# Kernel tuning notes

Measured on AMD Instinct MI355X. Metric: run time of the kernel, lower is better.

The kernel has to match this reference:

```python
import jax, jax.numpy as jnp
import numpy as np

NQ = 8
N = 2 ** NQ
NCYC = 4
B = 8192
_POP = np.array([bin(i).count('1') for i in range(N)], dtype=np.float32)  # popcount per basis state
_CNOT = np.array([[1, 0, 0, 0], [0, 1, 0, 0], [0, 0, 0, 1], [0, 0, 1, 0]], dtype=np.complex64)
_I4 = np.eye(4, dtype=np.complex64)
_XX = np.fliplr(np.eye(4)).astype(np.complex64)  # X (x) X in the 2-qubit basis


def _apply1(psi, U, w):
    # single-qubit gate U (2x2) on wire w; psi: (B, 256)
    b = psi.shape[0]
    s = psi.reshape(b, 1 << w, 2, -1)
    return jnp.einsum('ij,bljr->blir', U, s).reshape(b, N)


def _apply2_adj_b(psi, U, w):
    # batched 4x4 gate U (B,4,4) on adjacent wires (w, w+1)
    b = psi.shape[0]
    s = psi.reshape(b, 1 << w, 4, -1)
    return jnp.einsum('bij,bljr->blir', U, s).reshape(b, N)


def _apply2(psi, U, w0, w1):
    # fixed 4x4 gate on arbitrary wires (w0, w1)
    b = psi.shape[0]
    t = psi.reshape((b,) + (2,) * NQ)
    t = jnp.tensordot(jnp.asarray(U).reshape(2, 2, 2, 2), t, axes=((2, 3), (w0 + 1, w1 + 1)))
    t = jnp.moveaxis(t, (0, 1), (w0 + 1, w1 + 1))
    return t.reshape(b, N)


def _rz_mat(t):
    e = jnp.exp(-0.5j * t)
    return jnp.diag(jnp.stack([e, jnp.conj(e)])).astype(jnp.complex64)


def _ry_mat(t):
    c = jnp.cos(0.5 * t)
    s = jnp.sin(0.5 * t)
    return jnp.stack([jnp.stack([c, -s]), jnp.stack([s, c])]).astype(jnp.complex64)


def _u3_mat(p):
    th, ph, la = p[0], p[1], p[2]
    cc = jnp.cos(0.5 * th).astype(jnp.complex64)
    ss = jnp.sin(0.5 * th).astype(jnp.complex64)
    r0 = jnp.stack([cc, -jnp.exp(1j * la) * ss])
    r1 = jnp.stack([jnp.exp(1j * ph) * ss, jnp.exp(1j * (ph + la)) * cc])
    return jnp.stack([r0, r1]).astype(jnp.complex64)


def _expz(psi, w):
    # <Z_w> = p(bit=0) - p(bit=1)
    b = psi.shape[0]
    p = jnp.abs(psi.reshape(b, 1 << w, 2, -1)) ** 2
    m = p.sum(axis=(1, 3))
    return m[:, 0] - m[:, 1]


def _conv(psi, rz3, ry2, wq, wp):
    # RZ(wq) CNOT(wq,wp) RZ(wp) RY(wq) CNOT(wp,wq) RY(wq) CNOT(wq,wp) RZ(wp)
    psi = _apply1(psi, _rz_mat(rz3[0]), wq)
    psi = _apply2(psi, _CNOT, wq, wp)
    psi = _apply1(psi, _rz_mat(rz3[1]), wp)
    psi = _apply1(psi, _ry_mat(ry2[0]), wq)
    psi = _apply2(psi, _CNOT, wp, wq)
    psi = _apply1(psi, _ry_mat(ry2[1]), wq)
    psi = _apply2(psi, _CNOT, wq, wp)
    psi = _apply1(psi, _rz_mat(rz3[2]), wp)
    return psi


def setup_inputs() -> dict:
    key = jax.random.key(0)
    ks = jax.random.split(key, 8)
    pi = np.float32(np.pi)
    theta = jax.random.uniform(ks[0], (B,), jnp.float32, 0.0, pi / 2)
    phi = jax.random.uniform(ks[1], (B,), jnp.float32, 0.0, pi / 2)
    rz_params = jax.random.uniform(ks[2], (21,), jnp.float32, -pi, pi)
    ry_params = jax.random.uniform(ks[3], (14,), jnp.float32, -pi, pi)
    u3_params = jax.random.uniform(ks[4], (6, 3), jnp.float32, -pi, pi)
    w1 = jax.random.normal(ks[5], (10, 2), jnp.float32) / np.sqrt(2.0).astype(np.float32)
    b1 = jnp.zeros((10,), jnp.float32)
    w2 = jax.random.normal(ks[6], (1, 10), jnp.float32) / np.sqrt(10.0).astype(np.float32)
    b2 = jnp.zeros((1,), jnp.float32)
    return {'theta': theta, 'phi': phi, 'rz_params': rz_params, 'ry_params': ry_params,
            'u3_params': u3_params, 'w1': w1, 'b1': b1, 'w2': w2, 'b2': b2}


def reference(theta, phi, rz_params, ry_params, u3_params, w1, b1, w2, b2):
    b = theta.shape[0]
    # H on every wire from |0...0> -> uniform amplitudes 1/sqrt(2^8)
    psi = jnp.full((b, N), np.float32(2.0 ** (-NQ / 2)), dtype=jnp.complex64)
    # rz(2*phi) on all 8 wires == diagonal phase exp(i*phi*(2*popcount - 8))
    zphase = jnp.exp(1j * phi[:, None] * (2.0 * _POP[None, :] - NQ)).astype(jnp.complex64)
    # rxx(2*theta): cos(theta) I - i sin(theta) XX, batched over angles
    c = jnp.cos(theta)
    s = jnp.sin(theta)
    Urxx = (c[:, None, None] * _I4 - 1j * s[:, None, None] * _XX).astype(jnp.complex64)
    for _ in range(NCYC):
        psi = psi * zphase
        for w in (0, 2, 4, 6):  # pairs (0,1),(2,3),(4,5),(6,7)
            psi = _apply2_adj_b(psi, Urxx, w)
        for w in (1, 3, 5):  # pairs (1,2),(3,4),(5,6)
            psi = _apply2_adj_b(psi, Urxx, w)
    # first conv layer on pairs (1,0),(3,2),(5,4),(7,6)
    for i, (wq, wp) in enumerate([(1, 0), (3, 2), (5, 4), (7, 6)]):
        psi = _conv(psi, rz_params[3 * i:3 * i + 3], ry_params[2 * i:2 * i + 2], wq, wp)
    # U3 pooling on wires 1,3,5,7
    for i, w in enumerate((1, 3, 5, 7)):
        psi = _apply1(psi, _u3_mat(u3_params[i]), w)
    # second conv layer on pairs (3,1),(7,5),(5,3)
    for j, (wq, wp) in enumerate([(3, 1), (7, 5), (5, 3)]):
        i = 4 + j
        psi = _conv(psi, rz_params[3 * i:3 * i + 3], ry_params[2 * i:2 * i + 2], wq, wp)
    psi = _apply1(psi, _u3_mat(u3_params[4]), 3)
    psi = _apply1(psi, _u3_mat(u3_params[5]), 7)
    feats = jnp.stack([_expz(psi, 3), _expz(psi, 7)], axis=-1)  # (B, 2)
    h = jnp.tanh(feats @ w1.T + b1)
    return jax.nn.sigmoid(h @ w2.T + b2)  # (B, 1)
```

## Files before the change

kernel.cpp:

```cpp
#include <hip/hip_runtime.h>

typedef float2 cplx;

__device__ __forceinline__ cplx cmul(cplx a, cplx b){
  return make_float2(a.x*b.x - a.y*b.y, a.x*b.y + a.y*b.x);
}
__device__ __forceinline__ cplx cmad(cplx a, cplx b, cplx acc){
  return make_float2(acc.x + a.x*b.x - a.y*b.y, acc.y + a.x*b.y + a.y*b.x);
}

__device__ __forceinline__ void rz_gate(cplx* st, float t, int bmask){
  float s, c; sincosf(0.5f*t, &s, &c);
  cplx em = make_float2(c, -s), ep = make_float2(c, s);
  for(int k=0;k<4;k++) st[k] = cmul(st[k], (k & bmask) ? ep : em);
}
__device__ __forceinline__ void ry_gate_q(cplx* st, float t){
  float s, c; sincosf(0.5f*t, &s, &c);
  for(int bp=0;bp<2;bp++){
    cplx a0 = st[bp], a1 = st[2+bp];
    st[bp]   = make_float2(c*a0.x - s*a1.x, c*a0.y - s*a1.y);
    st[2+bp] = make_float2(s*a0.x + c*a1.x, s*a0.y + c*a1.y);
  }
}
__device__ __forceinline__ void u3_gate(cplx* st, const float* p, int onq){
  float th=p[0], ph=p[1], la=p[2];
  float ss,cc,sl,cl,sp,cp,spl,cpl;
  sincosf(0.5f*th,&ss,&cc); sincosf(la,&sl,&cl); sincosf(ph,&sp,&cp); sincosf(ph+la,&spl,&cpl);
  cplx u00=make_float2(cc,0.f), u01=make_float2(-cl*ss,-sl*ss);
  cplx u10=make_float2(cp*ss,sp*ss), u11=make_float2(cpl*cc,spl*cc);
  if(onq){
    for(int bp=0;bp<2;bp++){
      cplx a0=st[bp], a1=st[2+bp];
      st[bp]   = cmad(u01,a1,cmul(u00,a0));
      st[2+bp] = cmad(u11,a1,cmul(u10,a0));
    }
  } else {
    for(int bq=0;bq<2;bq++){
      cplx a0=st[2*bq], a1=st[2*bq+1];
      st[2*bq]   = cmad(u01,a1,cmul(u00,a0));
      st[2*bq+1] = cmad(u11,a1,cmul(u10,a0));
    }
  }
}


#define DPP_XOR1 0xB1
#define DPP_XOR2 0x4E
#define DPP_XOR3 0x1B
#define DPP_ROR8 0x128

template<int C>
__device__ __forceinline__ float xdpp(float x){
  return __builtin_bit_cast(float,
    __builtin_amdgcn_mov_dpp(__builtin_bit_cast(int, x), C, 0xF, 0xF, true));
}
template<int MASK>
__device__ __forceinline__ float xswz(float x){
  return __builtin_bit_cast(float,
    __builtin_amdgcn_ds_swizzle(__builtin_bit_cast(int, x), (MASK<<10) | 0x1F));
}

enum Sh { SH_DPP1, SH_DPP2, SH_DPP3, SH_ROR8, SH_SWZ4, SH_SWZ6, SH_SWZ10, SH_SWZ12 };

template<Sh S> __device__ __forceinline__ float shf(float x){
  if      constexpr(S==SH_DPP1)  return xdpp<DPP_XOR1>(x);
  else if constexpr(S==SH_DPP2)  return xdpp<DPP_XOR2>(x);
  else if constexpr(S==SH_DPP3)  return xdpp<DPP_XOR3>(x);
  else if constexpr(S==SH_ROR8)  return xdpp<DPP_ROR8>(x);
  else if constexpr(S==SH_SWZ4)  return xswz<4>(x);
  else if constexpr(S==SH_SWZ6)  return xswz<6>(x);
  else if constexpr(S==SH_SWZ10) return xswz<10>(x);
  else                           return xswz<12>(x);
}
template<Sh S> __device__ __forceinline__ cplx shc(cplx a){
  return make_float2(shf<S>(a.x), shf<S>(a.y));
}

template<int MR>
__device__ __forceinline__ void rxx_reg(cplx* v, float c, float s){
  #pragma unroll
  for(int r=0;r<16;r++){
    int q = r ^ MR;
    if(r > q) continue;
    cplx a = v[r], b = v[q];
    v[r] = make_float2(c*a.x + s*b.y, c*a.y - s*b.x);
    v[q] = make_float2(c*b.x + s*a.y, c*b.y - s*a.x);
  }
}
template<Sh S>
__device__ __forceinline__ void rxx_lane(cplx* v, float c, float s){
  #pragma unroll
  for(int r=0;r<16;r++){
    cplx p = shc<S>(v[r]);
    v[r] = make_float2(c*v[r].x + s*p.y, c*v[r].y - s*p.x);
  }
}
__device__ __forceinline__ void rxx_mix34(cplx* v, float c, float s){
  #pragma unroll
  for(int r=0;r<16;r+=2){
    cplx pa = shc<SH_DPP1>(v[r^1]);
    cplx pb = shc<SH_DPP1>(v[r]);
    cplx a = v[r], b = v[r^1];
    v[r]   = make_float2(c*a.x + s*pa.y, c*a.y - s*pa.x);
    v[r^1] = make_float2(c*b.x + s*pb.y, c*b.y - s*pb.x);
  }
}

template<int MQ, int MP>
__device__ __forceinline__ void conv_reg(cplx* v, const cplx* M){
  #pragma unroll
  for(int r=0;r<16;r++){
    if((r & (MQ|MP)) != 0) continue;
    cplx a0=v[r], a1=v[r^MP], a2=v[r^MQ], a3=v[r^MQ^MP];
    v[r]        = cmad(M[3], a3, cmad(M[2], a2, cmad(M[1], a1, cmul(M[0], a0))));
    v[r^MP]     = cmad(M[7], a3, cmad(M[6], a2, cmad(M[5], a1, cmul(M[4], a0))));
    v[r^MQ]     = cmad(M[11],a3, cmad(M[10],a2, cmad(M[9], a1, cmul(M[8], a0))));
    v[r^MQ^MP]  = cmad(M[15],a3, cmad(M[14],a2, cmad(M[13],a1, cmul(M[12],a0))));
  }
}

template<Sh SQ, Sh SP, Sh SB>
__device__ __forceinline__ void conv_lane(cplx* v, const cplx* M, int k){
  cplx es = M[k*4 + k], ep = M[k*4 + (k^1)], eq = M[k*4 + (k^2)], eb = M[k*4 + (k^3)];
  #pragma unroll
  for(int r=0;r<16;r++){
    cplx pq = shc<SQ>(v[r]);
    cplx pp = shc<SP>(v[r]);
    cplx pb = shc<SB>(v[r]);
    v[r] = cmad(eb, pb, cmad(eq, pq, cmad(ep, pp, cmul(es, v[r]))));
  }
}

__device__ __forceinline__ void conv_53(cplx* v, const cplx* M, int s1){
  int t = 2*s1, u = 2 - t;
  const cplx* r0 = M + t*4;
  const cplx* r1 = M + (t+1)*4;
  cplx e00=r0[t], e01=r0[t+1], e02=r0[u], e03=r0[u+1];
  cplx e10=r1[t], e11=r1[t+1], e12=r1[u], e13=r1[u+1];
  #pragma unroll
  for(int r=0;r<16;r+=2){
    cplx pv0 = shc<SH_DPP2>(v[r]);
    cplx pv1 = shc<SH_DPP2>(v[r+1]);
    cplx a0 = v[r], a1 = v[r+1];
    v[r]   = cmad(e03, pv1, cmad(e02, pv0, cmad(e01, a1, cmul(e00, a0))));
    v[r+1] = cmad(e13, pv1, cmad(e12, pv0, cmad(e11, a1, cmul(e10, a0))));
  }
}

__global__ void __launch_bounds__(256) qcnn_kernel(
    const float* __restrict__ theta, const float* __restrict__ phi,
    const float* __restrict__ rz, const float* __restrict__ ry,
    const float* __restrict__ u3,
    const float* __restrict__ w1, const float* __restrict__ b1,
    const float* __restrict__ w2, const float* __restrict__ b2,
    float* __restrict__ out){
  __shared__ cplx Msh[112];

  int tid  = threadIdx.x;

  if(tid < 28){
    int ci = tid >> 2, col = tid & 3;
    const float* rz3 = rz + 3*ci;
    const float* ry2 = ry + 2*ci;
    int u3slot = 0, u3idx = 0;
    if(ci <= 3){ u3slot = 1; u3idx = ci; }
    else if(ci == 5){ u3slot = 1; u3idx = 5; }
    else if(ci == 6){ u3slot = 2; u3idx = 4; }
    cplx st[4];
    for(int k=0;k<4;k++) st[k] = make_float2(k==col ? 1.f : 0.f, 0.f);
    rz_gate(st, rz3[0], 2);
    { cplx tmp=st[2]; st[2]=st[3]; st[3]=tmp; }
    rz_gate(st, rz3[1], 1);
    ry_gate_q(st, ry2[0]);
    { cplx tmp=st[1]; st[1]=st[3]; st[3]=tmp; }
    ry_gate_q(st, ry2[1]);
    { cplx tmp=st[2]; st[2]=st[3]; st[3]=tmp; }
    rz_gate(st, rz3[2], 1);
    if(u3slot == 1)      u3_gate(st, u3+3*u3idx, 1);
    else if(u3slot == 2) u3_gate(st, u3+3*u3idx, 0);
    for(int k=0;k<4;k++) Msh[ci*16 + k*4 + col] = st[k];
  }
  __syncthreads();

  int s_   = tid & 15;
  int b    = blockIdx.x*16 + (tid >> 4);
  int s0 = s_&1, s1 = (s_>>1)&1, s2 = (s_>>2)&1, s3 = (s_>>3)&1;

  float th = theta[b], ph = phi[b];
  float c, s;
  __sincosf(th, &s, &c);

  cplx zp[5];
  {
    int base = __popc(s_);
    float a0 = ph * (float)(2*base - 8);
    float sa, ca, s2p, c2p;
    __sincosf(a0, &sa, &ca);
    __sincosf(2.f*ph, &s2p, &c2p);
    cplx step = make_float2(c2p, s2p);
    zp[0] = make_float2(ca, sa);
    #pragma unroll
    for(int j=1;j<5;j++) zp[j] = cmul(zp[j-1], step);
  }

  cplx v[16];
  #pragma unroll
  for(int r=0;r<16;r++){
    cplx z = zp[__popc(r)];
    v[r] = make_float2(0.0625f*z.x, 0.0625f*z.y);
  }

  #pragma unroll 1
  for(int cyc=0;cyc<4;cyc++){
    if(cyc){
      #pragma unroll
      for(int r=0;r<16;r++) v[r] = cmul(v[r], zp[__popc(r)]);
    }
    rxx_reg<12>(v, c, s);
    rxx_reg<3>(v, c, s);
    rxx_lane<SH_DPP3>(v, c, s);
    rxx_lane<SH_SWZ12>(v, c, s);
    rxx_reg<6>(v, c, s);
    rxx_mix34(v, c, s);
    rxx_lane<SH_SWZ6>(v, c, s);
  }

  conv_reg<4,8>(v, Msh +  0);
  conv_reg<1,2>(v, Msh + 16);
  conv_lane<SH_DPP2,SH_DPP1,SH_DPP3>(v, Msh + 32, 2*s1 + s0);
  conv_lane<SH_ROR8,SH_SWZ4,SH_SWZ12>(v, Msh + 48, 2*s3 + s2);
  conv_reg<1,4>(v, Msh + 64);
  conv_lane<SH_ROR8,SH_DPP2,SH_SWZ10>(v, Msh + 80, 2*s3 + s1);
  conv_53(v, Msh + 96, s1);

  float tot = 0.f, z3 = 0.f;
  #pragma unroll
  for(int r=0;r<16;r++){
    float m = v[r].x*v[r].x + v[r].y*v[r].y;
    tot += m;
    z3 += (r & 1) ? -m : m;
  }
  float z7 = (s_ & 8) ? -tot : tot;
  z3 += xdpp<DPP_XOR1>(z3);  z7 += xdpp<DPP_XOR1>(z7);
  z3 += xdpp<DPP_XOR2>(z3);  z7 += xdpp<DPP_XOR2>(z7);
  z3 += xswz<4>(z3);         z7 += xswz<4>(z7);
  z3 += xdpp<DPP_ROR8>(z3);  z7 += xdpp<DPP_ROR8>(z7);

  float acc = 0.f;
  if(s_ < 10){
    float hv = tanhf(z3*w1[2*s_] + z7*w1[2*s_+1] + b1[s_]);
    acc = hv * w2[s_];
  }
  acc += xdpp<DPP_XOR1>(acc);
  acc += xdpp<DPP_XOR2>(acc);
  acc += xswz<4>(acc);
  acc += xdpp<DPP_ROR8>(acc);

  if(s_ == 0){
    float a = acc + b2[0];
    out[b] = 1.f / (1.f + __expf(-a));
  }
}

extern "C" void kernel_launch(void* const* d_in, const int* in_sizes, int n_in,
                              void* d_out, int out_size, void* d_ws, size_t ws_size,
                              hipStream_t stream) {
  const float* theta = (const float*)d_in[0];
  const float* phi   = (const float*)d_in[1];
  const float* rz    = (const float*)d_in[2];
  const float* ry    = (const float*)d_in[3];
  const float* u3    = (const float*)d_in[4];
  const float* w1    = (const float*)d_in[5];
  const float* b1    = (const float*)d_in[6];
  const float* w2    = (const float*)d_in[7];
  const float* b2    = (const float*)d_in[8];

  hipLaunchKernelGGL(qcnn_kernel, dim3(8192/16), dim3(256), 0, stream,
                     theta, phi, rz, ry, u3, w1, b1, w2, b2, (float*)d_out);
}
```

Measured before the change: 90.90 us.

## Use packed float2 vector math and replace ds_swizzle with chained DPP moves

Switches the complex type to a native two-float vector so the compiler can emit packed FMA instructions (v_pk_fma_f32) for the gate arithmetic. It also replaces every ds_swizzle cross-lane permutation with a composition of two DPP moves (quad permute followed by row mirror/half-mirror or rotate), so the shuffles avoid the LDS path. The DPP row modifiers address lanes differently from the xor swizzles, so the lane mapping must still give the same xor partners for correctness.

Result: no change. 90.07 us (-0.9%).

```diff
diff --git a/kernel.cpp b/kernel.cpp
--- a/kernel.cpp
+++ b/kernel.cpp
@@ -1,33 +1,40 @@
 #include <hip/hip_runtime.h>
 
-typedef float2 cplx;
-
+typedef float f32x2 __attribute__((ext_vector_type(2)));
+typedef f32x2 cplx;
+
+__device__ __forceinline__ cplx imul(cplx b){
+  cplx r = { -b[1], b[0] }; return r;
+}
 __device__ __forceinline__ cplx cmul(cplx a, cplx b){
-  return make_float2(a.x*b.x - a.y*b.y, a.x*b.y + a.y*b.x);
+  return a.xx*b + a.yy*imul(b);
 }
 __device__ __forceinline__ cplx cmad(cplx a, cplx b, cplx acc){
-  return make_float2(acc.x + a.x*b.x - a.y*b.y, acc.y + a.x*b.y + a.y*b.x);
+  return acc + a.xx*b + a.yy*imul(b);
+}
+__device__ __forceinline__ cplx rxx_upd(float c, cplx a, float s, cplx p){
+  return c*a - s*imul(p);
 }
 
 __device__ __forceinline__ void rz_gate(cplx* st, float t, int bmask){
   float s, c; sincosf(0.5f*t, &s, &c);
-  cplx em = make_float2(c, -s), ep = make_float2(c, s);
+  cplx em = {c, -s}, ep = {c, s};
   for(int k=0;k<4;k++) st[k] = cmul(st[k], (k & bmask) ? ep : em);
 }
 __device__ __forceinline__ void ry_gate_q(cplx* st, float t){
   float s, c; sincosf(0.5f*t, &s, &c);
   for(int bp=0;bp<2;bp++){
     cplx a0 = st[bp], a1 = st[2+bp];
-    st[bp]   = make_float2(c*a0.x - s*a1.x, c*a0.y - s*a1.y);
-    st[2+bp] = make_float2(s*a0.x + c*a1.x, s*a0.y + c*a1.y);
+    st[bp]   = c*a0 - s*a1;
+    st[2+bp] = s*a0 + c*a1;
   }
 }
 __device__ __forceinline__ void u3_gate(cplx* st, const float* p, int onq){
   float th=p[0], ph=p[1], la=p[2];
   float ss,cc,sl,cl,sp,cp,spl,cpl;
   sincosf(0.5f*th,&ss,&cc); sincosf(la,&sl,&cl); sincosf(ph,&sp,&cp); sincosf(ph+la,&spl,&cpl);
-  cplx u00=make_float2(cc,0.f), u01=make_float2(-cl*ss,-sl*ss);
-  cplx u10=make_float2(cp*ss,sp*ss), u11=make_float2(cpl*cc,spl*cc);
+  cplx u00={cc,0.f},      u01={-cl*ss,-sl*ss};
+  cplx u10={cp*ss,sp*ss}, u11={cpl*cc,spl*cc};
   if(onq){
     for(int bp=0;bp<2;bp++){
       cplx a0=st[bp], a1=st[2+bp];
@@ -48,16 +55,13 @@
 #define DPP_XOR2 0x4E
 #define DPP_XOR3 0x1B
 #define DPP_ROR8 0x128
+#define DPP_MIRR 0x140
+#define DPP_HALF 0x141
 
 template<int C>
 __device__ __forceinline__ float xdpp(float x){
   return __builtin_bit_cast(float,
     __builtin_amdgcn_mov_dpp(__builtin_bit_cast(int, x), C, 0xF, 0xF, true));
-}
-template<int MASK>
-__device__ __forceinline__ float xswz(float x){
-  return __builtin_bit_cast(float,
-    __builtin_amdgcn_ds_swizzle(__builtin_bit_cast(int, x), (MASK<<10) | 0x1F));
 }
 
 enum Sh { SH_DPP1, SH_DPP2, SH_DPP3, SH_ROR8, SH_SWZ4, SH_SWZ6, SH_SWZ10, SH_SWZ12 };
@@ -67,13 +71,13 @@
   else if constexpr(S==SH_DPP2)  return xdpp<DPP_XOR2>(x);
   else if constexpr(S==SH_DPP3)  return xdpp<DPP_XOR3>(x);
   else if constexpr(S==SH_ROR8)  return xdpp<DPP_ROR8>(x);
-  else if constexpr(S==SH_SWZ4)  return xswz<4>(x);
-  else if constexpr(S==SH_SWZ6)  return xswz<6>(x);
-  else if constexpr(S==SH_SWZ10) return xswz<10>(x);
-  else                           return xswz<12>(x);
+  else if constexpr(S==SH_SWZ4)  return xdpp<DPP_HALF>(xdpp<DPP_XOR3>(x));
+  else if constexpr(S==SH_SWZ6)  return xdpp<DPP_HALF>(xdpp<DPP_XOR1>(x));
+  else if constexpr(S==SH_SWZ10) return xdpp<DPP_ROR8>(xdpp<DPP_XOR2>(x));
+  else                           return xdpp<DPP_MIRR>(xdpp<DPP_XOR3>(x));
 }
 template<Sh S> __device__ __forceinline__ cplx shc(cplx a){
-  return make_float2(shf<S>(a.x), shf<S>(a.y));
+  cplx r; r[0] = shf<S>(a[0]); r[1] = shf<S>(a[1]); return r;
 }
 
 template<int MR>
@@ -83,8 +87,8 @@
     int q = r ^ MR;
     if(r > q) continue;
     cplx a = v[r], b = v[q];
-    v[r] = make_float2(c*a.x + s*b.y, c*a.y - s*b.x);
-    v[q] = make_float2(c*b.x + s*a.y, c*b.y - s*a.x);
+    v[r] = rxx_upd(c, a, s, b);
+    v[q] = rxx_upd(c, b, s, a);
   }
 }
 template<Sh S>
@@ -92,7 +96,7 @@
   #pragma unroll
   for(int r=0;r<16;r++){
     cplx p = shc<S>(v[r]);
-    v[r] = make_float2(c*v[r].x + s*p.y, c*v[r].y - s*p.x);
+    v[r] = rxx_upd(c, v[r], s, p);
   }
 }
 __device__ __forceinline__ void rxx_mix34(cplx* v, float c, float s){
@@ -101,8 +105,8 @@
     cplx pa = shc<SH_DPP1>(v[r^1]);
     cplx pb = shc<SH_DPP1>(v[r]);
     cplx a = v[r], b = v[r^1];
-    v[r]   = make_float2(c*a.x + s*pa.y, c*a.y - s*pa.x);
-    v[r^1] = make_float2(c*b.x + s*pb.y, c*b.y - s*pb.x);
+    v[r]   = rxx_upd(c, a, s, pa);
+    v[r^1] = rxx_upd(c, b, s, pb);
   }
 }
 
@@ -167,7 +171,7 @@
     else if(ci == 5){ u3slot = 1; u3idx = 5; }
     else if(ci == 6){ u3slot = 2; u3idx = 4; }
     cplx st[4];
-    for(int k=0;k<4;k++) st[k] = make_float2(k==col ? 1.f : 0.f, 0.f);
+    for(int k=0;k<4;k++){ cplx z = {k==col ? 1.f : 0.f, 0.f}; st[k] = z; }
     rz_gate(st, rz3[0], 2);
     { cplx tmp=st[2]; st[2]=st[3]; st[3]=tmp; }
     rz_gate(st, rz3[1], 1);
@@ -185,6 +189,7 @@
   int s_   = tid & 15;
   int b    = blockIdx.x*16 + (tid >> 4);
   int s0 = s_&1, s1 = (s_>>1)&1, s2 = (s_>>2)&1, s3 = (s_>>3)&1;
+  (void)s2;
 
   float th = theta[b], ph = phi[b];
   float c, s;
@@ -197,18 +202,16 @@
     float sa, ca, s2p, c2p;
     __sincosf(a0, &sa, &ca);
     __sincosf(2.f*ph, &s2p, &c2p);
-    cplx step = make_float2(c2p, s2p);
-    zp[0] = make_float2(ca, sa);
+    cplx step = {c2p, s2p};
+    cplx z0 = {ca, sa};
+    zp[0] = z0;
     #pragma unroll
     for(int j=1;j<5;j++) zp[j] = cmul(zp[j-1], step);
   }
 
   cplx v[16];
   #pragma unroll
-  for(int r=0;r<16;r++){
-    cplx z = zp[__popc(r)];
-    v[r] = make_float2(0.0625f*z.x, 0.0625f*z.y);
-  }
+  for(int r=0;r<16;r++) v[r] = 0.0625f * zp[__popc(r)];
 
   #pragma unroll 1
   for(int cyc=0;cyc<4;cyc++){
@@ -236,14 +239,15 @@
   float tot = 0.f, z3 = 0.f;
   #pragma unroll
   for(int r=0;r<16;r++){
-    float m = v[r].x*v[r].x + v[r].y*v[r].y;
+    f32x2 q = v[r]*v[r];
+    float m = q[0] + q[1];
     tot += m;
     z3 += (r & 1) ? -m : m;
   }
   float z7 = (s_ & 8) ? -tot : tot;
   z3 += xdpp<DPP_XOR1>(z3);  z7 += xdpp<DPP_XOR1>(z7);
   z3 += xdpp<DPP_XOR2>(z3);  z7 += xdpp<DPP_XOR2>(z7);
-  z3 += xswz<4>(z3);         z7 += xswz<4>(z7);
+  z3 += xdpp<DPP_HALF>(z3);  z7 += xdpp<DPP_HALF>(z7);
   z3 += xdpp<DPP_ROR8>(z3);  z7 += xdpp<DPP_ROR8>(z7);
 
   float acc = 0.f;
@@ -253,7 +257,7 @@
   }
   acc += xdpp<DPP_XOR1>(acc);
   acc += xdpp<DPP_XOR2>(acc);
-  acc += xswz<4>(acc);
+  acc += xdpp<DPP_HALF>(acc);
   acc += xdpp<DPP_ROR8>(acc);
 
   if(s_ == 0){
```
